# Performance work log

Measured on AMD Instinct MI355X. Metric: run time of the kernel, lower is better.

## Reference

```python
import jax, jax.numpy as jnp
import numpy as np

N0, N1, N2 = 400000, 75000, 15000
E1, E2 = 1200000, 240000
F_IN, NC = 64, 40
H1, C1 = 2, 8          # layer 1: heads=2, out_channels=8 -> concat dim 16
H2, C2 = 1, NC         # layer 2: heads=1, out_channels=num_classes
NEG_SLOPE = 0.2


def gat_conv(x_src, x_dst, src, dst, Ws, Wd, att_s, att_d, bias, heads, ch):
    """PyG GATConv on bipartite (x_src, x_dst) with remove+add self loops."""
    n_dst = x_dst.shape[0]
    hs = (x_src @ Ws).reshape(-1, heads, ch)   # [N_src, H, C]
    hd = (x_dst @ Wd).reshape(-1, heads, ch)   # [N_dst, H, C]
    a_s = (hs * att_s).sum(-1)                 # [N_src, H]
    a_d = (hd * att_d).sum(-1)                 # [N_dst, H]
    loops = jnp.arange(n_dst)
    src_all = jnp.concatenate([src, loops])
    dst_all = jnp.concatenate([dst, loops])
    # remove_self_loops: drop pre-existing i->i edges; add_self_loops: appended
    valid = jnp.concatenate([src != dst, jnp.ones(n_dst, dtype=bool)])[:, None]
    logits = jax.nn.leaky_relu(a_s[src_all] + a_d[dst_all], NEG_SLOPE)  # [E, H]
    logits = jnp.where(valid, logits, -jnp.inf)
    m = jax.ops.segment_max(logits, dst_all, num_segments=n_dst)        # [N_dst, H]
    w = jnp.where(valid, jnp.exp(logits - m[dst_all]), 0.0)
    denom = jax.ops.segment_sum(w, dst_all, num_segments=n_dst)
    alpha = w / denom[dst_all]                                          # [E, H]
    out = jax.ops.segment_sum(alpha[:, :, None] * hs[src_all], dst_all,
                              num_segments=n_dst)                       # [N_dst, H, C]
    return out.reshape(n_dst, heads * ch) + bias


def setup_inputs() -> dict:
    key = jax.random.key(0)
    ks = jax.random.split(key, 16)
    s = 0.1
    return {
        "x": jax.random.normal(ks[0], (N0, F_IN), dtype=jnp.float32),
        "e1_src": jax.random.randint(ks[1], (E1,), 0, N0),
        "e1_dst": jax.random.randint(ks[2], (E1,), 0, N1),
        "e2_src": jax.random.randint(ks[3], (E2,), 0, N1),
        "e2_dst": jax.random.randint(ks[4], (E2,), 0, N2),
        "W1s": jax.random.normal(ks[5], (F_IN, H1 * C1), dtype=jnp.float32) * s,
        "W1d": jax.random.normal(ks[6], (F_IN, H1 * C1), dtype=jnp.float32) * s,
        "att1_s": jax.random.normal(ks[7], (H1, C1), dtype=jnp.float32) * s,
        "att1_d": jax.random.normal(ks[8], (H1, C1), dtype=jnp.float32) * s,
        "b1": jnp.zeros((H1 * C1,), dtype=jnp.float32),
        "W2s": jax.random.normal(ks[9], (H1 * C1, H2 * C2), dtype=jnp.float32) * s,
        "W2d": jax.random.normal(ks[10], (H1 * C1, H2 * C2), dtype=jnp.float32) * s,
        "att2_s": jax.random.normal(ks[11], (H2, C2), dtype=jnp.float32) * s,
        "att2_d": jax.random.normal(ks[12], (H2, C2), dtype=jnp.float32) * s,
        "b2": jnp.zeros((H2 * C2,), dtype=jnp.float32),
    }


def reference(x, e1_src, e1_dst, e2_src, e2_dst,
              W1s, W1d, att1_s, att1_d, b1,
              W2s, W2d, att2_s, att2_d, b2):
    h = gat_conv(x, x[:N1], e1_src, e1_dst, W1s, W1d, att1_s, att1_d, b1, H1, C1)
    h = jax.nn.elu(h)
    o = gat_conv(h, h[:N2], e2_src, e2_dst, W2s, W2d, att2_s, att2_d, b2, H2, C2)
    return jax.nn.log_softmax(o, axis=-1)
```

## Files before the change

### kernel.cpp

```cpp
#include <hip/hip_runtime.h>
#include <hip/hip_bf16.h>

constexpr int N0 = 400000, N1 = 75000, N2 = 15000;
constexpr int E1 = 1200000, E2 = 240000;
constexpr int NC = 40;
constexpr float NEG_SLOPE = 0.2f;

constexpr int BK1 = 128;
constexpr int NB1 = (N1 + BK1 - 1) / BK1;
constexpr int CAPB1 = 2432;
constexpr int BK2 = 32;
constexpr int NB2 = (N2 + BK2 - 1) / BK2;
constexpr int CAPB2 = 704;

constexpr int TILE = 8192;
constexpr int NT1 = (E1 + TILE - 1) / TILE;
constexpr int NT2 = (E2 + TILE - 1) / TILE;
constexpr int BPJ = (N0 + 511) / 512;

using f32x4 = __attribute__((ext_vector_type(4))) float;
using s16x8 = __attribute__((ext_vector_type(8))) short;

__device__ __forceinline__ float leaky(float v) { return v > 0.f ? v : NEG_SLOPE * v; }

__device__ __forceinline__ unsigned cvtpk(float lo, float hi) {
    unsigned r;
    asm("v_cvt_pk_bf16_f32 %0, %1, %2" : "=v"(r) : "v"(lo), "v"(hi));
    return r;
}

__device__ __forceinline__ unsigned bf16pair(float lo, float hi) {
    unsigned a = __float_as_uint(lo), b = __float_as_uint(hi);
    a = (a + 0x7FFFu + ((a >> 16) & 1u)) >> 16;
    b = (b + 0x7FFFu + ((b >> 16) & 1u)) & 0xFFFF0000u;
    return a | b;
}
__device__ __forceinline__ float bfLo(unsigned w) { return __uint_as_float(w << 16); }
__device__ __forceinline__ float bfHi(unsigned w) { return __uint_as_float(w & 0xFFFF0000u); }

__global__ __launch_bounds__(256, 4) void k1_kernel(
    const float* __restrict__ x,
    const float* __restrict__ W1s, const float* __restrict__ W1d,
    const float* __restrict__ att1s, const float* __restrict__ att1d,
    const int* __restrict__ e1s, const int* __restrict__ e1d,
    const int* __restrict__ e2s, const int* __restrict__ e2d,
    unsigned* __restrict__ rec1, float* __restrict__ a_d1,
    int* __restrict__ gcnt1, unsigned* __restrict__ bin1,
    int* __restrict__ gcnt2, unsigned* __restrict__ bin2)
{
    __shared__ int hist[NB1];
    __shared__ int gbase[NB1];
    __shared__ float2 vds[64];

    int bid = blockIdx.x;
    const int tid = threadIdx.x;
    if (bid < NT1 + NT2) {
        const bool isL1 = bid < NT1;
        const int* es = isL1 ? e1s : e2s;
        const int* ed = isL1 ? e1d : e2d;
        const int nE = isL1 ? E1 : E2;
        const int nb = isL1 ? NB1 : NB2;
        const int cap = isL1 ? CAPB1 : CAPB2;
        const int shift = isL1 ? 7 : 5;
        const int lsh = isL1 ? 19 : 17;
        int* gc = isL1 ? gcnt1 : gcnt2;
        unsigned* gbin = isL1 ? bin1 : bin2;
        const int base = (isL1 ? bid : bid - NT1) * TILE;
        const int lim = min(TILE, nE - base);

        for (int b = tid; b < nb; b += 256) hist[b] = 0;
        __syncthreads();
        for (int i = tid; i < lim; i += 256) {
            int s = es[base + i], d = ed[base + i];
            if (s != d) atomicAdd(&hist[d >> shift], 1);
        }
        __syncthreads();
        for (int b = tid; b < nb; b += 256) {
            int c = hist[b];
            gbase[b] = (c > 0) ? atomicAdd(&gc[b], c) : 0;
            hist[b] = 0;
        }
        __syncthreads();
        for (int i = tid; i < lim; i += 256) {
            int s = es[base + i], d = ed[base + i];
            if (s != d) {
                int b = d >> shift;
                int pos = gbase[b] + atomicAdd(&hist[b], 1);
                if (pos < cap)
                    gbin[(size_t)b * cap + pos] =
                        (unsigned)s | ((unsigned)(d & ((1 << shift) - 1)) << lsh);
            }
        }
        return;
    }
    bid -= NT1 + NT2;
    const int l    = tid & 63;
    const int nd   = l & 15;
    const int kg   = l >> 4;
    const int wv   = tid >> 6;
    const int nodeBase = bid * 512;
    const bool hasN1 = nodeBase < N1;

    if (hasN1) {
        if (tid < 64) {
            float d0 = 0.f, d1 = 0.f;
            const float* wr = W1d + (size_t)tid * 16;
            #pragma unroll
            for (int cc = 0; cc < 8; ++cc) {
                d0 = fmaf(wr[cc], att1d[cc], d0);
                d1 = fmaf(wr[8 + cc], att1d[8 + cc], d1);
            }
            vds[tid] = make_float2(d0, d1);
        }
        __syncthreads();
    }

    s16x8 bf0, bf1;
    {
        union { unsigned u[4]; s16x8 v; } t0, t1;
        #pragma unroll
        for (int q = 0; q < 4; ++q) {
            t0.u[q] = cvtpk(W1s[(8 * kg + 2 * q) * 16 + nd],
                            W1s[(8 * kg + 2 * q + 1) * 16 + nd]);
            t1.u[q] = cvtpk(W1s[(32 + 8 * kg + 2 * q) * 16 + nd],
                            W1s[(32 + 8 * kg + 2 * q + 1) * 16 + nd]);
        }
        bf0 = t0.v; bf1 = t1.v;
    }
    float att4[4];
    #pragma unroll
    for (int r = 0; r < 4; ++r) att4[r] = att1s[4 * kg + r];

    const int myBase = nodeBase + wv * 16 + nd;

    float4 A0, A1, A2, A3, B0, B1, B2, B3, C0, C1, C2, C3;

    auto LOADr = [&](int r, float4& q0, float4& q1, float4& q2, float4& q3) {
        int n = min(myBase + r * 64, N0 - 1);
        const float* xr_ = x + (size_t)n * 64 + 8 * kg;
        q0 = *(const float4*)(xr_);
        q1 = *(const float4*)(xr_ + 4);
        q2 = *(const float4*)(xr_ + 32);
        q3 = *(const float4*)(xr_ + 36);
    };
    auto COMPUTEr = [&](int r, float4& p0, float4& p1, float4& p2, float4& p3) {
        const int node = myBase + r * 64;
        union { unsigned u[4]; s16x8 v; } a0, a1;
        a0.u[0] = cvtpk(p0.x, p0.y); a0.u[1] = cvtpk(p0.z, p0.w);
        a0.u[2] = cvtpk(p1.x, p1.y); a0.u[3] = cvtpk(p1.z, p1.w);
        a1.u[0] = cvtpk(p2.x, p2.y); a1.u[1] = cvtpk(p2.z, p2.w);
        a1.u[2] = cvtpk(p3.x, p3.y); a1.u[3] = cvtpk(p3.z, p3.w);

        f32x4 acc = {0.f, 0.f, 0.f, 0.f};
        acc = __builtin_amdgcn_mfma_f32_16x16x32_bf16(bf0, a0.v, acc, 0, 0, 0);
        acc = __builtin_amdgcn_mfma_f32_16x16x32_bf16(bf1, a1.v, acc, 0, 0, 0);

        float p = acc[0] * att4[0];
        p = fmaf(acc[1], att4[1], p);
        p = fmaf(acc[2], att4[2], p);
        p = fmaf(acc[3], att4[3], p);
        p += __shfl_xor(p, 16, 64);
        float q = __shfl_xor(p, 32, 64);

        if (node < N0) {
            unsigned* rp = rec1 + (size_t)node * 16;
            uint2 hw;
            hw.x = cvtpk(acc[0], acc[1]);
            hw.y = cvtpk(acc[2], acc[3]);
            *(uint2*)(rp + 2 * kg) = hw;
            if (kg == 0)
                *(uint4*)(rp + 8) = make_uint4(__float_as_uint(p), __float_as_uint(q), 0u, 0u);
            else if (kg == 1)
                *(uint4*)(rp + 12) = make_uint4(0u, 0u, 0u, 0u);
        }
        if (hasN1 && node < N1) {
            float xv8[16] = {p0.x, p0.y, p0.z, p0.w, p1.x, p1.y, p1.z, p1.w,
                             p2.x, p2.y, p2.z, p2.w, p3.x, p3.y, p3.z, p3.w};
            float d0 = 0.f, d1 = 0.f;
            #pragma unroll
            for (int j = 0; j < 8; ++j) {
                float2 v = vds[8 * kg + j];
                d0 = fmaf(xv8[j], v.x, d0);
                d1 = fmaf(xv8[j], v.y, d1);
            }
            #pragma unroll
            for (int j = 0; j < 8; ++j) {
                float2 v = vds[32 + 8 * kg + j];
                d0 = fmaf(xv8[8 + j], v.x, d0);
                d1 = fmaf(xv8[8 + j], v.y, d1);
            }
            d0 += __shfl_xor(d0, 16, 64); d0 += __shfl_xor(d0, 32, 64);
            d1 += __shfl_xor(d1, 16, 64); d1 += __shfl_xor(d1, 32, 64);
            if (kg == 0)
                ((float2*)a_d1)[node] = make_float2(d0, d1);
        }
    };

    LOADr(0, A0, A1, A2, A3);
    LOADr(1, B0, B1, B2, B3);
    LOADr(2, C0, C1, C2, C3);  COMPUTEr(0, A0, A1, A2, A3);
    LOADr(3, A0, A1, A2, A3);  COMPUTEr(1, B0, B1, B2, B3);
    LOADr(4, B0, B1, B2, B3);  COMPUTEr(2, C0, C1, C2, C3);
    LOADr(5, C0, C1, C2, C3);  COMPUTEr(3, A0, A1, A2, A3);
    LOADr(6, A0, A1, A2, A3);  COMPUTEr(4, B0, B1, B2, B3);
    LOADr(7, B0, B1, B2, B3);  COMPUTEr(5, C0, C1, C2, C3);
    COMPUTEr(6, A0, A1, A2, A3);
    COMPUTEr(7, B0, B1, B2, B3);
}

__global__ __launch_bounds__(512) void k2_kernel(
    const int* __restrict__ gcnt1, const unsigned* __restrict__ bin1,
    const unsigned* __restrict__ rec1, const float* __restrict__ a_d1,
    const float* __restrict__ b1,
    const float* __restrict__ W2s, const float* __restrict__ W2d,
    const float* __restrict__ att2s, const float* __restrict__ att2d,
    unsigned* __restrict__ rec2)
{
    __shared__ unsigned srt[CAPB1];
    __shared__ int hist[BK1], start[BK1 + 1];
    __shared__ float w2sl[640], va[16], vd[16];
    __shared__ float h1s[BK1][17];

    const int b = blockIdx.x, tid = threadIdx.x;
    const int d0 = b * BK1;
    const int nN = min(BK1, N1 - d0);
    const int ncnt = min(gcnt1[b], CAPB1);
    const unsigned* bp = bin1 + (size_t)b * CAPB1;

    for (int i = tid; i < 640; i += 512) w2sl[i] = W2s[i];
    if (tid < BK1) hist[tid] = 0;
    if (tid >= 128 && tid < 144) {
        int k = tid - 128;
        float sa = 0.f, sd = 0.f;
        for (int cc = 0; cc < 40; ++cc) {
            sa = fmaf(W2s[k * 40 + cc], att2s[cc], sa);
            sd = fmaf(W2d[k * 40 + cc], att2d[cc], sd);
        }
        va[k] = sa; vd[k] = sd;
    }
    __syncthreads();
    for (int i = tid; i < ncnt; i += 512) atomicAdd(&hist[bp[i] >> 19], 1);
    __syncthreads();
    if (tid == 0) {
        int a = 0;
        for (int k = 0; k < BK1; ++k) { start[k] = a; a += hist[k]; }
        start[BK1] = a;
    }
    __syncthreads();
    if (tid < BK1) hist[tid] = start[tid];
    __syncthreads();
    for (int i = tid; i < ncnt; i += 512) {
        unsigned p = bp[i];
        int pos = atomicAdd(&hist[p >> 19], 1);
        srt[pos] = p & 0x7FFFFu;
    }
    __syncthreads();

    const int g = tid >> 4, c = tid & 15, h = c >> 3;
    const int wbase = tid & 48;
    const int wmap = (c < 8) ? c : (8 + ((c >> 2) & 1));
    for (int n = g; n < nN; n += 32) {
        const int node = d0 + n;
        const float ad = a_d1[(size_t)node * 2 + h];
        const int st = start[n], cnt = start[n + 1] - start[n];
        unsigned rw0 = rec1[(size_t)node * 16 + wmap];
        unsigned rw1 = (cnt >= 1) ? rec1[(size_t)srt[st] * 16 + wmap] : 0u;
        unsigned rw2 = (cnt >= 2) ? rec1[(size_t)srt[st + 1] * 16 + wmap] : 0u;
        unsigned rw3 = (cnt >= 3) ? rec1[(size_t)srt[st + 2] * 16 + wmap] : 0u;
        float accv = 0.f, den = 0.f;
        for (int j = 0; j <= cnt; ++j) {
            float asv = __uint_as_float((unsigned)__shfl((int)rw0, wbase + 8 + 4 * h, 64));
            unsigned chw = (unsigned)__shfl((int)rw0, wbase + (c >> 1), 64);
            float hv = (c & 1) ? bfHi(chw) : bfLo(chw);
            float w = __expf(leaky(asv + ad));
            accv = fmaf(w, hv, accv);
            den += w;
            rw0 = rw1; rw1 = rw2; rw2 = rw3;
            rw3 = (j + 4 <= cnt) ? rec1[(size_t)srt[st + j + 3] * 16 + wmap] : 0u;
        }
        float v = accv / den + b1[c];
        h1s[n][c] = v > 0.f ? v : (__expf(v) - 1.f);
    }
    __syncthreads();
    for (int i = tid; i < nN * 24; i += 512) {
        int nn = i / 24, w = i - nn * 24;
        unsigned* rp = rec2 + (size_t)(d0 + nn) * 24;
        if (w < 20) {
            int c0 = 2 * w, c1 = c0 + 1;
            float s0 = 0.f, s1 = 0.f;
            #pragma unroll
            for (int k = 0; k < 16; ++k) {
                float hk = h1s[nn][k];
                s0 = fmaf(hk, w2sl[k * 40 + c0], s0);
                s1 = fmaf(hk, w2sl[k * 40 + c1], s1);
            }
            rp[w] = bf16pair(s0, s1);
        } else if (w < 22) {
            const float* vv = (w == 20) ? va : vd;
            float s = 0.f;
            #pragma unroll
            for (int k = 0; k < 16; ++k) s = fmaf(h1s[nn][k], vv[k], s);
            rp[w] = __float_as_uint(s);
        }
    }
}

__global__ __launch_bounds__(1024) void k3_kernel(
    const int* __restrict__ gcnt2, const unsigned* __restrict__ bin2,
    const unsigned* __restrict__ rec2, const float* __restrict__ b2,
    float* __restrict__ out)
{
    __shared__ unsigned srt[CAPB2];
    __shared__ int hist[BK2], start[BK2 + 1];

    const int b = blockIdx.x, tid = threadIdx.x;
    const int d0 = b * BK2;
    const int nN = min(BK2, N2 - d0);
    const int ncnt = min(gcnt2[b], CAPB2);
    const unsigned* bp = bin2 + (size_t)b * CAPB2;

    if (tid < BK2) hist[tid] = 0;
    __syncthreads();
    for (int i = tid; i < ncnt; i += 1024) atomicAdd(&hist[bp[i] >> 17], 1);
    __syncthreads();
    if (tid == 0) {
        int a = 0;
        for (int k = 0; k < BK2; ++k) { start[k] = a; a += hist[k]; }
        start[BK2] = a;
    }
    __syncthreads();
    if (tid < BK2) hist[tid] = start[tid];
    __syncthreads();
    for (int i = tid; i < ncnt; i += 1024) {
        unsigned p = bp[i];
        int pos = atomicAdd(&hist[p >> 17], 1);
        srt[pos] = p & 0x1FFFFu;
    }
    __syncthreads();

    const int g = tid >> 5, l = tid & 31;
    const float bb0 = (l < 20) ? b2[2 * l] : 0.f;
    const float bb1 = (l < 20) ? b2[2 * l + 1] : 0.f;
    for (int n = g; n < nN; n += 32) {
        const int node = d0 + n;
        const int st = start[n], cnt = start[n + 1] - start[n];
        unsigned rw0 = (l < 22) ? rec2[(size_t)node * 24 + l] : 0u;
        const float ad = __uint_as_float((unsigned)__shfl((int)rw0, 21, 32));
        unsigned rw1 = (cnt >= 1 && l < 21) ? rec2[(size_t)srt[st] * 24 + l] : 0u;
        unsigned rw2 = (cnt >= 2 && l < 21) ? rec2[(size_t)srt[st + 1] * 24 + l] : 0u;
        unsigned rw3 = (cnt >= 3 && l < 21) ? rec2[(size_t)srt[st + 2] * 24 + l] : 0u;
        float a0 = 0.f, a1 = 0.f, den = 0.f;
        for (int j = 0; j <= cnt; ++j) {
            float asv = __uint_as_float((unsigned)__shfl((int)rw0, 20, 32));
            float w = __expf(leaky(asv + ad));
            a0 = fmaf(w, bfLo(rw0), a0);
            a1 = fmaf(w, bfHi(rw0), a1);
            den += w;
            rw0 = rw1; rw1 = rw2; rw2 = rw3;
            rw3 = (j + 4 <= cnt && l < 21) ? rec2[(size_t)srt[st + j + 3] * 24 + l] : 0u;
        }
        float v0 = (l < 20) ? a0 / den + bb0 : -3.4e38f;
        float v1 = (l < 20) ? a1 / den + bb1 : -3.4e38f;
        float mx = fmaxf(v0, v1);
        #pragma unroll
        for (int k = 16; k >= 1; k >>= 1) mx = fmaxf(mx, __shfl_xor(mx, k, 32));
        float ex = (l < 20) ? __expf(v0 - mx) + __expf(v1 - mx) : 0.f;
        #pragma unroll
        for (int k = 16; k >= 1; k >>= 1) ex += __shfl_xor(ex, k, 32);
        float lse = mx + logf(ex);
        if (l < 20)
            ((float2*)(out + (size_t)node * 40))[l] = make_float2(v0 - lse, v1 - lse);
    }
}

extern "C" void kernel_launch(void* const* d_in, const int* in_sizes, int n_in,
                              void* d_out, int out_size, void* d_ws, size_t ws_size,
                              hipStream_t stream) {
    const float* x      = (const float*)d_in[0];
    const int*   e1_src = (const int*)d_in[1];
    const int*   e1_dst = (const int*)d_in[2];
    const int*   e2_src = (const int*)d_in[3];
    const int*   e2_dst = (const int*)d_in[4];
    const float* W1s    = (const float*)d_in[5];
    const float* W1d    = (const float*)d_in[6];
    const float* att1s  = (const float*)d_in[7];
    const float* att1d  = (const float*)d_in[8];
    const float* b1     = (const float*)d_in[9];
    const float* W2s    = (const float*)d_in[10];
    const float* W2d    = (const float*)d_in[11];
    const float* att2s  = (const float*)d_in[12];
    const float* att2d  = (const float*)d_in[13];
    const float* b2     = (const float*)d_in[14];
    float* out = (float*)d_out;

    float* wsbase = (float*)d_ws;
    size_t o = 0;
    int*      gcnt1 = (int*)(wsbase + o);      o += NB1;
    int*      gcnt2 = (int*)(wsbase + o);      o += NB2;
    const size_t zeroWords = o;
    unsigned* bin1  = (unsigned*)(wsbase + o); o += (size_t)NB1 * CAPB1;
    unsigned* bin2  = (unsigned*)(wsbase + o); o += (size_t)NB2 * CAPB2;
    unsigned* rec1  = (unsigned*)(wsbase + o); o += (size_t)N0 * 16;
    float*    a_d1  = (float*)(wsbase + o);    o += (size_t)N1 * 2;
    unsigned* rec2  = (unsigned*)(wsbase + o); o += (size_t)N1 * 24;

    hipMemsetAsync(d_ws, 0, zeroWords * sizeof(float), stream);

    k1_kernel<<<NT1 + NT2 + BPJ, 256, 0, stream>>>(
        x, W1s, W1d, att1s, att1d, e1_src, e1_dst, e2_src, e2_dst,
        rec1, a_d1, gcnt1, bin1, gcnt2, bin2);

    k2_kernel<<<NB1, 512, 0, stream>>>(gcnt1, bin1, rec1, a_d1, b1,
                                       W2s, W2d, att2s, att2d, rec2);

    k3_kernel<<<NB2, 1024, 0, stream>>>(gcnt2, bin2, rec2, b2, out);
}
```

Measured before the change: 120.3 us.

## Split edge binning and projection into separate kernels; deepen x prefetch pipeline

The fused k1 kernel is split into k1a, which bins edges by destination, and k1b, which runs the layer-1 projection MFMA, and the two are launched back to back. In k1b the rolling three-stage load rotation becomes a four-deep prefetch. The a_d dot product is computed before the next load reuses the registers, and a sched_barrier pins the ordering. This is meant to cut register pressure and shared-memory use for the projection blocks and hide more of the x load latency. The cost is an extra launch, the binning work and the projection no longer overlapping in one grid, and occupancy dropping from 4 to 2 blocks per SIMD under the launch bounds.

```diff
diff --git a/kernel.cpp b/kernel.cpp
--- a/kernel.cpp
+++ b/kernel.cpp
@@ -38,67 +38,65 @@
 __device__ __forceinline__ float bfLo(unsigned w) { return __uint_as_float(w << 16); }
 __device__ __forceinline__ float bfHi(unsigned w) { return __uint_as_float(w & 0xFFFF0000u); }
 
-__global__ __launch_bounds__(256, 4) void k1_kernel(
-    const float* __restrict__ x,
-    const float* __restrict__ W1s, const float* __restrict__ W1d,
-    const float* __restrict__ att1s, const float* __restrict__ att1d,
+__global__ __launch_bounds__(256) void k1a_kernel(
     const int* __restrict__ e1s, const int* __restrict__ e1d,
     const int* __restrict__ e2s, const int* __restrict__ e2d,
-    unsigned* __restrict__ rec1, float* __restrict__ a_d1,
     int* __restrict__ gcnt1, unsigned* __restrict__ bin1,
     int* __restrict__ gcnt2, unsigned* __restrict__ bin2)
 {
     __shared__ int hist[NB1];
     __shared__ int gbase[NB1];
+
+    const int bid = blockIdx.x;
+    const int tid = threadIdx.x;
+    const bool isL1 = bid < NT1;
+    const int* es = isL1 ? e1s : e2s;
+    const int* ed = isL1 ? e1d : e2d;
+    const int nE = isL1 ? E1 : E2;
+    const int nb = isL1 ? NB1 : NB2;
+    const int cap = isL1 ? CAPB1 : CAPB2;
+    const int shift = isL1 ? 7 : 5;
+    const int lsh = isL1 ? 19 : 17;
+    int* gc = isL1 ? gcnt1 : gcnt2;
+    unsigned* gbin = isL1 ? bin1 : bin2;
+    const int base = (isL1 ? bid : bid - NT1) * TILE;
+    const int lim = min(TILE, nE - base);
+
+    for (int b = tid; b < nb; b += 256) hist[b] = 0;
+    __syncthreads();
+    for (int i = tid; i < lim; i += 256) {
+        int s = es[base + i], d = ed[base + i];
+        if (s != d) atomicAdd(&hist[d >> shift], 1);
+    }
+    __syncthreads();
+    for (int b = tid; b < nb; b += 256) {
+        int c = hist[b];
+        gbase[b] = (c > 0) ? atomicAdd(&gc[b], c) : 0;
+        hist[b] = 0;
+    }
+    __syncthreads();
+    for (int i = tid; i < lim; i += 256) {
+        int s = es[base + i], d = ed[base + i];
+        if (s != d) {
+            int b = d >> shift;
+            int pos = gbase[b] + atomicAdd(&hist[b], 1);
+            if (pos < cap)
+                gbin[(size_t)b * cap + pos] =
+                    (unsigned)s | ((unsigned)(d & ((1 << shift) - 1)) << lsh);
+        }
+    }
+}
+
+__global__ __launch_bounds__(256, 2) void k1b_kernel(
+    const float* __restrict__ x,
+    const float* __restrict__ W1s, const float* __restrict__ W1d,
+    const float* __restrict__ att1s, const float* __restrict__ att1d,
+    unsigned* __restrict__ rec1, float* __restrict__ a_d1)
+{
     __shared__ float2 vds[64];
-
-    int bid = blockIdx.x;
     const int tid = threadIdx.x;
-    if (bid < NT1 + NT2) {
-        const bool isL1 = bid < NT1;
-        const int* es = isL1 ? e1s : e2s;
-        const int* ed = isL1 ? e1d : e2d;
-        const int nE = isL1 ? E1 : E2;
-        const int nb = isL1 ? NB1 : NB2;
-        const int cap = isL1 ? CAPB1 : CAPB2;
-        const int shift = isL1 ? 7 : 5;
-        const int lsh = isL1 ? 19 : 17;
-        int* gc = isL1 ? gcnt1 : gcnt2;
-        unsigned* gbin = isL1 ? bin1 : bin2;
-        const int base = (isL1 ? bid : bid - NT1) * TILE;
-        const int lim = min(TILE, nE - base);
-
-        for (int b = tid; b < nb; b += 256) hist[b] = 0;
-        __syncthreads();
-        for (int i = tid; i < lim; i += 256) {
-            int s = es[base + i], d = ed[base + i];
-            if (s != d) atomicAdd(&hist[d >> shift], 1);
-        }
-        __syncthreads();
-        for (int b = tid; b < nb; b += 256) {
-            int c = hist[b];
-            gbase[b] = (c > 0) ? atomicAdd(&gc[b], c) : 0;
-            hist[b] = 0;
-        }
-        __syncthreads();
-        for (int i = tid; i < lim; i += 256) {
-            int s = es[base + i], d = ed[base + i];
-            if (s != d) {
-                int b = d >> shift;
-                int pos = gbase[b] + atomicAdd(&hist[b], 1);
-                if (pos < cap)
-                    gbin[(size_t)b * cap + pos] =
-                        (unsigned)s | ((unsigned)(d & ((1 << shift) - 1)) << lsh);
-            }
-        }
-        return;
-    }
-    bid -= NT1 + NT2;
-    const int l    = tid & 63;
-    const int nd   = l & 15;
-    const int kg   = l >> 4;
-    const int wv   = tid >> 6;
-    const int nodeBase = bid * 512;
+    const int l = tid & 63, nd = l & 15, kg = l >> 4, wv = tid >> 6;
+    const int nodeBase = blockIdx.x * 512;
     const bool hasN1 = nodeBase < N1;
 
     if (hasN1) {
@@ -133,23 +131,51 @@
 
     const int myBase = nodeBase + wv * 16 + nd;
 
-    float4 A0, A1, A2, A3, B0, B1, B2, B3, C0, C1, C2, C3;
-
-    auto LOADr = [&](int r, float4& q0, float4& q1, float4& q2, float4& q3) {
+    float4 P[4][4];
+
+    auto LOADr = [&](int r, float4 (&Q)[4]) {
         int n = min(myBase + r * 64, N0 - 1);
         const float* xr_ = x + (size_t)n * 64 + 8 * kg;
-        q0 = *(const float4*)(xr_);
-        q1 = *(const float4*)(xr_ + 4);
-        q2 = *(const float4*)(xr_ + 32);
-        q3 = *(const float4*)(xr_ + 36);
+        Q[0] = *(const float4*)(xr_);
+        Q[1] = *(const float4*)(xr_ + 4);
+        Q[2] = *(const float4*)(xr_ + 32);
+        Q[3] = *(const float4*)(xr_ + 36);
     };
-    auto COMPUTEr = [&](int r, float4& p0, float4& p1, float4& p2, float4& p3) {
+
+    #pragma unroll
+    for (int r = 0; r < 4; ++r) LOADr(r, P[r]);
+
+    #pragma unroll
+    for (int r = 0; r < 8; ++r) {
         const int node = myBase + r * 64;
+        float4 (&Q)[4] = P[r & 3];
+
         union { unsigned u[4]; s16x8 v; } a0, a1;
-        a0.u[0] = cvtpk(p0.x, p0.y); a0.u[1] = cvtpk(p0.z, p0.w);
-        a0.u[2] = cvtpk(p1.x, p1.y); a0.u[3] = cvtpk(p1.z, p1.w);
-        a1.u[0] = cvtpk(p2.x, p2.y); a1.u[1] = cvtpk(p2.z, p2.w);
-        a1.u[2] = cvtpk(p3.x, p3.y); a1.u[3] = cvtpk(p3.z, p3.w);
+        a0.u[0] = cvtpk(Q[0].x, Q[0].y); a0.u[1] = cvtpk(Q[0].z, Q[0].w);
+        a0.u[2] = cvtpk(Q[1].x, Q[1].y); a0.u[3] = cvtpk(Q[1].z, Q[1].w);
+        a1.u[0] = cvtpk(Q[2].x, Q[2].y); a1.u[1] = cvtpk(Q[2].z, Q[2].w);
+        a1.u[2] = cvtpk(Q[3].x, Q[3].y); a1.u[3] = cvtpk(Q[3].z, Q[3].w);
+
+        float pd0 = 0.f, pd1 = 0.f;
+        if (hasN1) {
+            float xv8[16] = {Q[0].x, Q[0].y, Q[0].z, Q[0].w, Q[1].x, Q[1].y, Q[1].z, Q[1].w,
+                             Q[2].x, Q[2].y, Q[2].z, Q[2].w, Q[3].x, Q[3].y, Q[3].z, Q[3].w};
+            #pragma unroll
+            for (int j = 0; j < 8; ++j) {
+                float2 v = vds[8 * kg + j];
+                pd0 = fmaf(xv8[j], v.x, pd0);
+                pd1 = fmaf(xv8[j], v.y, pd1);
+            }
+            #pragma unroll
+            for (int j = 0; j < 8; ++j) {
+                float2 v = vds[32 + 8 * kg + j];
+                pd0 = fmaf(xv8[8 + j], v.x, pd0);
+                pd1 = fmaf(xv8[8 + j], v.y, pd1);
+            }
+        }
+
+        if (r + 4 < 8) LOADr(r + 4, Q);
+        __builtin_amdgcn_sched_barrier(0);
 
         f32x4 acc = {0.f, 0.f, 0.f, 0.f};
         acc = __builtin_amdgcn_mfma_f32_16x16x32_bf16(bf0, a0.v, acc, 0, 0, 0);
@@ -174,38 +200,12 @@
                 *(uint4*)(rp + 12) = make_uint4(0u, 0u, 0u, 0u);
         }
         if (hasN1 && node < N1) {
-            float xv8[16] = {p0.x, p0.y, p0.z, p0.w, p1.x, p1.y, p1.z, p1.w,
-                             p2.x, p2.y, p2.z, p2.w, p3.x, p3.y, p3.z, p3.w};
-            float d0 = 0.f, d1 = 0.f;
-            #pragma unroll
-            for (int j = 0; j < 8; ++j) {
-                float2 v = vds[8 * kg + j];
-                d0 = fmaf(xv8[j], v.x, d0);
-                d1 = fmaf(xv8[j], v.y, d1);
-            }
-            #pragma unroll
-            for (int j = 0; j < 8; ++j) {
-                float2 v = vds[32 + 8 * kg + j];
-                d0 = fmaf(xv8[8 + j], v.x, d0);
-                d1 = fmaf(xv8[8 + j], v.y, d1);
-            }
-            d0 += __shfl_xor(d0, 16, 64); d0 += __shfl_xor(d0, 32, 64);
-            d1 += __shfl_xor(d1, 16, 64); d1 += __shfl_xor(d1, 32, 64);
+            pd0 += __shfl_xor(pd0, 16, 64); pd0 += __shfl_xor(pd0, 32, 64);
+            pd1 += __shfl_xor(pd1, 16, 64); pd1 += __shfl_xor(pd1, 32, 64);
             if (kg == 0)
-                ((float2*)a_d1)[node] = make_float2(d0, d1);
-        }
-    };
-
-    LOADr(0, A0, A1, A2, A3);
-    LOADr(1, B0, B1, B2, B3);
-    LOADr(2, C0, C1, C2, C3);  COMPUTEr(0, A0, A1, A2, A3);
-    LOADr(3, A0, A1, A2, A3);  COMPUTEr(1, B0, B1, B2, B3);
-    LOADr(4, B0, B1, B2, B3);  COMPUTEr(2, C0, C1, C2, C3);
-    LOADr(5, C0, C1, C2, C3);  COMPUTEr(3, A0, A1, A2, A3);
-    LOADr(6, A0, A1, A2, A3);  COMPUTEr(4, B0, B1, B2, B3);
-    LOADr(7, B0, B1, B2, B3);  COMPUTEr(5, C0, C1, C2, C3);
-    COMPUTEr(6, A0, A1, A2, A3);
-    COMPUTEr(7, B0, B1, B2, B3);
+                ((float2*)a_d1)[node] = make_float2(pd0, pd1);
+        }
+    }
 }
 
 __global__ __launch_bounds__(512) void k2_kernel(
@@ -406,9 +406,11 @@
 
     hipMemsetAsync(d_ws, 0, zeroWords * sizeof(float), stream);
 
-    k1_kernel<<<NT1 + NT2 + BPJ, 256, 0, stream>>>(
-        x, W1s, W1d, att1s, att1d, e1_src, e1_dst, e2_src, e2_dst,
-        rec1, a_d1, gcnt1, bin1, gcnt2, bin2);
+    k1a_kernel<<<NT1 + NT2, 256, 0, stream>>>(
+        e1_src, e1_dst, e2_src, e2_dst, gcnt1, bin1, gcnt2, bin2);
+
+    k1b_kernel<<<BPJ, 256, 0, stream>>>(
+        x, W1s, W1d, att1s, att1d, rec1, a_d1);
 
     k2_kernel<<<NB1, 512, 0, stream>>>(gcnt1, bin1, rec1, a_d1, b1,
                                        W2s, W2d, att2s, att2d, rec2);
```

Measured after the change: 133.9 us. +11.3%, slower.
